# Performance work log

Hardware: AMD Instinct MI355X
Metric: run time of the kernel (lower is better)

The kernel has to match this reference:

```python
import jax, jax.numpy as jnp
import numpy as np

EPS = 1e-8

def setup_inputs() -> dict:
    key = jax.random.key(0)
    k1, k2, k3 = jax.random.split(key, 3)
    b, c, h, w = 64, 20, 128, 128
    x = jax.random.normal(k1, (b, c, h, w), dtype=jnp.float32)
    y = jax.random.randint(k2, (b, c), 0, 2).astype(jnp.int32)
    threshold_p = jnp.zeros((b, c, h * w), dtype=jnp.float32)
    fg = jax.random.uniform(k3, (b, c), dtype=jnp.float32)
    return {"x": x, "y": y, "threshold_p": threshold_p, "fg": fg, "iter": 0}

def reference(x, y, threshold_p, fg, iter):
    b, c, h, w = x.shape
    hw = h * w
    xs = jax.nn.sigmoid(x.reshape(b, c, hw))  # [b,c,hw]
    yf = y.astype(xs.dtype)
    if iter % 100 < 80:
        # per-row descending sort, pick the fg*(h*w)-th value as threshold
        srt = -jnp.sort(-xs.reshape(b * c, hw), axis=1)  # descending
        idx = (fg.reshape(-1) * hw).astype(jnp.int32)  # [b*c]
        thr = jnp.take_along_axis(srt, idx[:, None], axis=1).reshape(b, c, 1)
        thr = jax.lax.stop_gradient(thr)
    else:
        thr = jax.nn.sigmoid(jnp.mean(threshold_p.reshape(b, c, hw), axis=2))[:, :, None]
        xs = jax.lax.stop_gradient(xs)
    thr = jnp.clip(thr, 0.0001)  # [b,c,1], broadcasts over hw
    y_ = yf[:, :, None]  # [b,c,1] broadcast equivalent of stacking hw copies
    mask_low = jax.lax.stop_gradient((xs <= thr).astype(xs.dtype) * y_)
    mask_high = jax.lax.stop_gradient((xs > thr).astype(xs.dtype) * y_)
    h_low = (-(xs * xs) / (thr * thr) + 2.0 * xs / thr) * mask_low
    alpha = 1.0 / jnp.clip((1.0 - thr) ** 2, EPS)
    h_high = alpha * (1.0 - xs) * (1.0 - 2.0 * thr + xs) * mask_high
    if iter % 100 < 80:
        neg_loss = -(1.0 - y_) * jnp.log(jnp.clip(1.0 - xs, EPS))
        loss = jnp.mean(h_high + h_low + neg_loss)
    else:
        loss = jnp.sum(h_low) / jnp.sum(mask_low) + jnp.sum(h_high) / jnp.sum(mask_high)
    return loss
```

## Files before the change

### kernel.cpp

```cpp
#include <hip/hip_runtime.h>

#define HW     16384
#define NROWS  1280
#define NT     512
#define NWAVES (NT / 64)
#define CAP    1536
#define MAXB   128

__device__ __forceinline__ unsigned f2u(float f) {
    unsigned u = __float_as_uint(f);
    unsigned m = (unsigned)((int)u >> 31);
    return u ^ (m | 0x80000000u);
}
__device__ __forceinline__ float u2f(unsigned u) {
    u = (u & 0x80000000u) ? (u & 0x7fffffffu) : ~u;
    return __uint_as_float(u);
}

__device__ __forceinline__ float norminv(float p) {
    const float a1=-3.969683028665376e+01f,a2=2.209460984245205e+02f,
                a3=-2.759285104469687e+02f,a4=1.383577518672690e+02f,
                a5=-3.066479806614716e+01f,a6=2.506628277459239e+00f;
    const float b1=-5.447609879822406e+01f,b2=1.615858368580409e+02f,
                b3=-1.556989798598866e+02f,b4=6.680131188771972e+01f,
                b5=-1.328068155288572e+01f;
    const float c1=-7.784894002430293e-03f,c2=-3.223964580411365e-01f,
                c3=-2.400758277161838e+00f,c4=-2.549732539343734e+00f,
                c5=4.374664141464968e+00f,c6=2.938163982698783e+00f;
    const float d1=7.784695709041462e-03f,d2=3.224671290700398e-01f,
                d3=2.445134137142996e+00f,d4=3.754408661907416e+00f;
    const float plow = 0.02425f;
    float q, r;
    if (p < plow) {
        q = sqrtf(-2.f * logf(p));
        return (((((c1*q+c2)*q+c3)*q+c4)*q+c5)*q+c6) /
               ((((d1*q+d2)*q+d3)*q+d4)*q+1.f);
    } else if (p <= 1.f - plow) {
        q = p - 0.5f; r = q * q;
        return (((((a1*r+a2)*r+a3)*r+a4)*r+a5)*r+a6)*q /
               (((((b1*r+b2)*r+b3)*r+b4)*r+b5)*r+1.f);
    } else {
        q = sqrtf(-2.f * logf(1.f - p));
        return -(((((c1*q+c2)*q+c3)*q+c4)*q+c5)*q+c6) /
                ((((d1*q+d2)*q+d3)*q+d4)*q+1.f);
    }
}

__device__ __forceinline__ void block_scan_pick(
    const unsigned* h, int bpl, unsigned kk,
    volatile unsigned* s_bin, volatile unsigned* s_k, unsigned* wtot)
{
    const int tid  = threadIdx.x;
    const int lane = tid & 63;
    const int wid  = tid >> 6;
    const int base = tid * bpl;
    unsigned local = 0;
    for (int j = 0; j < bpl; ++j) local += h[base + j];
    unsigned s = local;
    #pragma unroll
    for (int off = 1; off < 64; off <<= 1) {
        unsigned t = __shfl_down(s, off, 64);
        if (lane + off < 64) s += t;
    }
    if (lane == 0) wtot[wid] = s;
    __syncthreads();
    unsigned aw = 0;
    #pragma unroll
    for (int w = 0; w < NWAVES; ++w) if (w > wid) aw += wtot[w];
    const unsigned above = aw + (s - local);
    if (above <= kk && above + local > kk) {
        unsigned run = above;
        for (int j = bpl - 1; j >= 0; --j) {
            unsigned c = h[base + j];
            if (run + c > kk) { *s_bin = (unsigned)(base + j); *s_k = kk - run; break; }
            run += c;
        }
    }
    __syncthreads();
}

__global__ __launch_bounds__(NT) void spatial_bce_row(
    const float* __restrict__ x, const int* __restrict__ y,
    const float* __restrict__ fg, double* __restrict__ partial)
{
    __shared__ unsigned hist[4096];
    __shared__ unsigned buf[CAP];
    __shared__ unsigned buf2[MAXB];
    __shared__ unsigned wtot[NWAVES];
    __shared__ unsigned s_cnt, s_cnt2, s_bin, s_k, s_val;
    __shared__ float    swf[NWAVES][6];
    __shared__ double   swd[NWAVES];

    const int row  = blockIdx.x;
    const int tid  = threadIdx.x;
    const int lane = tid & 63;
    const int wid  = tid >> 6;
    const float4* x4 = (const float4*)(x + (size_t)row * HW);
    const float L2E   = 1.44269504f;
    const float LN2   = 0.69314718f;
    const float NLCAP = 18.420680744f;

    const int yrow = y[row];

    if (yrow == 0) {
        float a0 = 0.f, a1 = 0.f, a2 = 0.f, a3 = 0.f;
        for (int i = tid; i < HW / 4; i += NT) {
            float4 v = x4[i];
            a0 += fminf(fmaxf(v.x, 0.f) + LN2 * log2f(1.f + exp2f(-L2E * fabsf(v.x))), NLCAP);
            a1 += fminf(fmaxf(v.y, 0.f) + LN2 * log2f(1.f + exp2f(-L2E * fabsf(v.y))), NLCAP);
            a2 += fminf(fmaxf(v.z, 0.f) + LN2 * log2f(1.f + exp2f(-L2E * fabsf(v.z))), NLCAP);
            a3 += fminf(fmaxf(v.w, 0.f) + LN2 * log2f(1.f + exp2f(-L2E * fabsf(v.w))), NLCAP);
        }
        double acc = (double)((a0 + a1) + (a2 + a3));
        #pragma unroll
        for (int off = 32; off > 0; off >>= 1) acc += __shfl_down(acc, off, 64);
        if (lane == 0) swd[wid] = acc;
        __syncthreads();
        if (tid == 0) {
            double t = 0.0;
            for (int w = 0; w < NWAVES; ++w) t += swd[w];
            partial[row] = t;
        }
        return;
    }

    int k = (int)(fg[row] * (float)HW);
    k = max(0, min(HW - 1, k));
    const unsigned ku = (unsigned)k;
    const float pq  = 1.f - ((float)k + 0.5f) * (1.f / (float)HW);
    const float z   = norminv(pq);
    const float phi = 0.39894228f * exp2f(-0.72134752f * z * z);
    const float sig = sqrtf(pq * (1.f - pq) * (1.f / (float)HW)) / phi;
    const float dl  = 6.f * sig + 0.02f;
    const float fa  = z + dl, fb = z - dl;
    const unsigned ua = f2u(fa), ub = f2u(fb);

    {
        uint4 zz = {0u, 0u, 0u, 0u};
        for (int i = tid; i < 1024 / 4; i += NT) ((uint4*)hist)[i] = zz;
    }
    if (tid == 0) { s_cnt = 0u; s_cnt2 = 0u; }
    __syncthreads();

    float t1a = 0.f, t2a = 0.f, gaa = 0.f, g2aa = 0.f, cafa = 0.f, cbfa = 0.f;
    float t1b = 0.f, t2b = 0.f, gab = 0.f, g2ab = 0.f, cafb = 0.f, cbfb = 0.f;
    for (int i = tid; i < HW / 4; i += 2 * NT) {
        float4 v0 = x4[i];
        float4 v1 = x4[i + NT];
        float e0[4] = {v0.x, v0.y, v0.z, v0.w};
        float e1[4] = {v1.x, v1.y, v1.z, v1.w};
        #pragma unroll
        for (int j = 0; j < 4; ++j) {
            float xv = e0[j];
            unsigned u = f2u(xv);
            float s = __builtin_amdgcn_rcpf(1.f + exp2f(-L2E * xv));
            float s2 = s * s;
            t1a += s; t2a += s2;
            if (u > ua) { gaa += s; g2aa += s2; cafa += 1.f; }
            if (u > ub) {
                cbfa += 1.f;
                if (u <= ua) { unsigned p = atomicAdd(&s_cnt, 1u); if (p < CAP) buf[p] = u; }
            }
        }
        #pragma unroll
        for (int j = 0; j < 4; ++j) {
            float xv = e1[j];
            unsigned u = f2u(xv);
            float s = __builtin_amdgcn_rcpf(1.f + exp2f(-L2E * xv));
            float s2 = s * s;
            t1b += s; t2b += s2;
            if (u > ua) { gab += s; g2ab += s2; cafb += 1.f; }
            if (u > ub) {
                cbfb += 1.f;
                if (u <= ua) { unsigned p = atomicAdd(&s_cnt, 1u); if (p < CAP) buf[p] = u; }
            }
        }
    }
    float t1 = t1a + t1b, t2 = t2a + t2b;
    float ga = gaa + gab, g2a = g2aa + g2ab;
    float caf = cafa + cafb, cbf = cbfa + cbfb;
    #pragma unroll
    for (int off = 32; off > 0; off >>= 1) {
        t1  += __shfl_down(t1,  off, 64);
        t2  += __shfl_down(t2,  off, 64);
        ga  += __shfl_down(ga,  off, 64);
        g2a += __shfl_down(g2a, off, 64);
        caf += __shfl_down(caf, off, 64);
        cbf += __shfl_down(cbf, off, 64);
    }
    if (lane == 0) {
        swf[wid][0] = t1;  swf[wid][1] = t2;  swf[wid][2] = ga;
        swf[wid][3] = g2a; swf[wid][4] = caf; swf[wid][5] = cbf;
    }
    __syncthreads();
    double dS1 = 0, dS2 = 0, dGa = 0, dG2a = 0, dCa = 0, dCb = 0;
    #pragma unroll
    for (int w = 0; w < NWAVES; ++w) {
        dS1 += swf[w][0]; dS2 += swf[w][1]; dGa  += swf[w][2];
        dG2a += swf[w][3]; dCa += swf[w][4]; dCb += swf[w][5];
    }
    const unsigned ca  = (unsigned)(dCa + 0.5);
    const unsigned cb  = (unsigned)(dCb + 0.5);
    const unsigned cnt = s_cnt;
    const unsigned UCLIP = f2u(-9.2102404f);
    const bool valid = (ca <= ku) && (ku < cb) && (cnt <= CAP);

    unsigned ustar;
    bool addSide;
    float hs = 0.f, hs2 = 0.f, hn = 0.f;

    if (valid) {
        const float scale = 1024.f / (fa - fb);
        for (int c = tid; c < (int)cnt; c += NT) {
            float xv = u2f(buf[c]);
            int bn = (int)((xv - fb) * scale);
            bn = max(0, min(1023, bn));
            atomicAdd(&hist[bn], 1u);
        }
        __syncthreads();
        const unsigned kp = ku - ca;
        block_scan_pick(hist, 1024 / NT, kp, &s_bin, &s_k, wtot);
        const unsigned binv = s_bin;
        const unsigned kin  = s_k;
        for (int c = tid; c < (int)cnt; c += NT) {
            unsigned u = buf[c];
            float xv = u2f(u);
            int bn = (int)((xv - fb) * scale);
            bn = max(0, min(1023, bn));
            if (bn == (int)binv) { unsigned p = atomicAdd(&s_cnt2, 1u); if (p < MAXB) buf2[p] = u; }
        }
        __syncthreads();
        const unsigned m = s_cnt2;
        if (m <= MAXB) {
            for (int i = tid; i < (int)m; i += NT) {
                unsigned v = buf2[i];
                unsigned gt = 0, eq = 0;
                for (int j = 0; j < (int)m; ++j) {
                    unsigned w = buf2[j];
                    gt += (w > v); eq += (w == v);
                }
                if (gt <= kin && kin < gt + eq) s_val = v;
            }
        } else {
            for (int c = tid; c < (int)cnt; c += NT) {
                unsigned v = buf[c];
                unsigned gt = 0, eq = 0;
                for (int j = 0; j < (int)cnt; ++j) {
                    unsigned w = buf[j];
                    gt += (w > v); eq += (w == v);
                }
                if (gt <= kp && kp < gt + eq) s_val = v;
            }
        }
        __syncthreads();
        ustar = s_val;

        if (ustar >= UCLIP) {
            addSide = true;
            for (int c = tid; c < (int)cnt; c += NT) {
                unsigned u = buf[c];
                if (u > ustar) {
                    float xv = u2f(u);
                    float s = __builtin_amdgcn_rcpf(1.f + exp2f(-L2E * xv));
                    hs += s; hs2 += s * s; hn += 1.f;
                }
            }
        } else {
            addSide = false;
            for (int i = tid; i < HW / 4; i += NT) {
                float4 v = x4[i];
                float e[4] = {v.x, v.y, v.z, v.w};
                #pragma unroll
                for (int j = 0; j < 4; ++j) {
                    if (f2u(e[j]) > UCLIP) {
                        float s = __builtin_amdgcn_rcpf(1.f + exp2f(-L2E * e[j]));
                        hs += s; hs2 += s * s; hn += 1.f;
                    }
                }
            }
        }
    } else {
        {
            uint4 zz = {0u, 0u, 0u, 0u};
            for (int i = tid; i < 4096 / 4; i += NT) ((uint4*)hist)[i] = zz;
        }
        __syncthreads();
        for (int i = tid; i < HW / 4; i += NT) {
            float4 v = x4[i];
            atomicAdd(&hist[f2u(v.x) >> 20], 1u);
            atomicAdd(&hist[f2u(v.y) >> 20], 1u);
            atomicAdd(&hist[f2u(v.z) >> 20], 1u);
            atomicAdd(&hist[f2u(v.w) >> 20], 1u);
        }
        __syncthreads();
        block_scan_pick(hist, 4096 / NT, ku, &s_bin, &s_k, wtot);
        const unsigned bin1 = s_bin;
        const unsigned k1   = s_k;
        for (int i = tid; i < 2048; i += NT) hist[i] = 0u;
        __syncthreads();
        for (int i = tid; i < HW / 4; i += NT) {
            float4 v = x4[i];
            unsigned u[4] = {f2u(v.x), f2u(v.y), f2u(v.z), f2u(v.w)};
            #pragma unroll
            for (int j = 0; j < 4; ++j)
                if ((u[j] >> 20) == bin1) atomicAdd(&hist[(u[j] >> 10) & 1023u], 1u);
        }
        __syncthreads();
        block_scan_pick(hist, 1024 / NT, k1, &s_bin, &s_k, wtot);
        const unsigned pfx22 = (bin1 << 10) | s_bin;
        const unsigned k2    = s_k;
        for (int i = tid; i < HW / 4; i += NT) {
            float4 v = x4[i];
            unsigned u[4] = {f2u(v.x), f2u(v.y), f2u(v.z), f2u(v.w)};
            #pragma unroll
            for (int j = 0; j < 4; ++j)
                if ((u[j] >> 10) == pfx22) atomicAdd(&hist[1024 + (u[j] & 1023u)], 1u);
        }
        __syncthreads();
        block_scan_pick(hist + 1024, 1024 / NT, k2, &s_bin, &s_k, wtot);
        ustar = (pfx22 << 10) | s_bin;

        addSide = false;
        const unsigned uthr = max(ustar, UCLIP);
        for (int i = tid; i < HW / 4; i += NT) {
            float4 v = x4[i];
            float e[4] = {v.x, v.y, v.z, v.w};
            #pragma unroll
            for (int j = 0; j < 4; ++j) {
                if (f2u(e[j]) > uthr) {
                    float s = __builtin_amdgcn_rcpf(1.f + exp2f(-L2E * e[j]));
                    hs += s; hs2 += s * s; hn += 1.f;
                }
            }
        }
    }

    #pragma unroll
    for (int off = 32; off > 0; off >>= 1) {
        hs  += __shfl_down(hs,  off, 64);
        hs2 += __shfl_down(hs2, off, 64);
        hn  += __shfl_down(hn,  off, 64);
    }
    if (lane == 0) { swf[wid][0] = hs; swf[wid][1] = hs2; swf[wid][2] = hn; }
    __syncthreads();
    if (tid == 0) {
        double HS = 0, HS2 = 0, HN = 0;
        for (int w = 0; w < NWAVES; ++w) {
            HS += swf[w][0]; HS2 += swf[w][1]; HN += swf[w][2];
        }
        double SH, S2H, NH;
        if (addSide) { SH = dGa + HS; S2H = dG2a + HS2; NH = dCa + HN; }
        else         { SH = HS;       S2H = HS2;        NH = HN; }
        const double SL = dS1 - SH, S2L = dS2 - S2H;

        const float xk = u2f(ustar);
        float thrf = 1.0f / (1.0f + expf(-xk));
        thrf = fmaxf(thrf, 1e-4f);
        const double t   = (double)thrf;
        const double omt = 1.0 - t;
        const double al  = 1.0 / fmax(omt * omt, 1e-8);
        partial[row] = 2.0 * SL / t - S2L / (t * t)
                     + al * (NH * (1.0 - 2.0 * t) + 2.0 * t * SH - S2H);
    }
}

__global__ __launch_bounds__(256) void spatial_bce_final(
    const double* __restrict__ partial, float* __restrict__ out)
{
    __shared__ double sred[256];
    double acc = 0.0;
    for (int i = threadIdx.x; i < NROWS; i += 256) acc += partial[i];
    sred[threadIdx.x] = acc;
    __syncthreads();
    for (int off = 128; off > 0; off >>= 1) {
        if (threadIdx.x < off) sred[threadIdx.x] += sred[threadIdx.x + off];
        __syncthreads();
    }
    if (threadIdx.x == 0)
        out[0] = (float)(sred[0] / ((double)NROWS * (double)HW));
}

extern "C" void kernel_launch(void* const* d_in, const int* in_sizes, int n_in,
                              void* d_out, int out_size, void* d_ws, size_t ws_size,
                              hipStream_t stream) {
    const float* x  = (const float*)d_in[0];
    const int*   y  = (const int*)d_in[1];
    const float* fg = (const float*)d_in[3];

    double* partial = (double*)d_ws;

    spatial_bce_row<<<NROWS, NT, 0, stream>>>(x, y, fg, partial);
    spatial_bce_final<<<1, 256, 0, stream>>>(partial, (float*)d_out);
}
```

Measured before the change: 38.38 us.

## Fuse final reduction into row kernel via last-block atomic, shrink blocks and shared memory

Measured after the change: 65.05 us. 69.5% more time.

```diff
diff --git a/kernel.cpp b/kernel.cpp
--- a/kernel.cpp
+++ b/kernel.cpp
@@ -2,10 +2,9 @@
 
 #define HW     16384
 #define NROWS  1280
-#define NT     512
-#define NWAVES (NT / 64)
-#define CAP    1536
-#define MAXB   128
+#define NT     256
+#define CAP    2048
+#define MB     256
 
 __device__ __forceinline__ unsigned f2u(float f) {
     unsigned u = __float_as_uint(f);
@@ -46,6 +45,15 @@
     }
 }
 
+__device__ __forceinline__ void bracket_ab(int k, float* fa, float* fb) {
+    const float pq  = 1.f - ((float)k + 0.5f) * (1.f / (float)HW);
+    const float z   = norminv(pq);
+    const float phi = 0.39894228f * exp2f(-0.72134752f * z * z);
+    const float sig = sqrtf(pq * (1.f - pq) * (1.f / (float)HW)) / phi;
+    const float dl  = 6.f * sig + 0.02f;
+    *fa = z + dl; *fb = z - dl;
+}
+
 __device__ __forceinline__ void block_scan_pick(
     const unsigned* h, int bpl, unsigned kk,
     volatile unsigned* s_bin, volatile unsigned* s_k, unsigned* wtot)
@@ -66,7 +74,7 @@
     __syncthreads();
     unsigned aw = 0;
     #pragma unroll
-    for (int w = 0; w < NWAVES; ++w) if (w > wid) aw += wtot[w];
+    for (int w = 0; w < 4; ++w) if (w > wid) aw += wtot[w];
     const unsigned above = aw + (s - local);
     if (above <= kk && above + local > kk) {
         unsigned run = above;
@@ -79,17 +87,17 @@
     __syncthreads();
 }
 
-__global__ __launch_bounds__(NT) void spatial_bce_row(
+__global__ __launch_bounds__(NT, 8) void fused_all(
     const float* __restrict__ x, const int* __restrict__ y,
-    const float* __restrict__ fg, double* __restrict__ partial)
+    const float* __restrict__ fg, double* __restrict__ partial,
+    unsigned* __restrict__ done, float* __restrict__ out)
 {
-    __shared__ unsigned hist[4096];
-    __shared__ unsigned buf[CAP];
-    __shared__ unsigned buf2[MAXB];
-    __shared__ unsigned wtot[NWAVES];
-    __shared__ unsigned s_cnt, s_cnt2, s_bin, s_k, s_val;
-    __shared__ float    swf[NWAVES][6];
-    __shared__ double   swd[NWAVES];
+    __shared__ __align__(16) unsigned pool[4096];
+    __shared__ unsigned wtot[4];
+    __shared__ unsigned s_cnt, s_cnt2, s_bin, s_k, s_val, s_last;
+    __shared__ float    swf[4][6];
+    __shared__ double   smom[6];
+    __shared__ double   swd[4];
 
     const int row  = blockIdx.x;
     const int tid  = threadIdx.x;
@@ -116,268 +124,238 @@
         for (int off = 32; off > 0; off >>= 1) acc += __shfl_down(acc, off, 64);
         if (lane == 0) swd[wid] = acc;
         __syncthreads();
+        if (tid == 0) partial[row] = swd[0] + swd[1] + swd[2] + swd[3];
+    } else {
+        int k = (int)(fg[row] * (float)HW);
+        k = max(0, min(HW - 1, k));
+        const unsigned ku = (unsigned)k;
+        float fa, fb; bracket_ab(k, &fa, &fb);
+        const unsigned ua = f2u(fa), ub = f2u(fb);
+        const unsigned UCLIP = f2u(-9.2102404f);
+
+        for (int i = tid; i < 1024; i += NT) pool[2048 + i] = 0u;
+        if (tid == 0) { s_cnt = 0u; s_cnt2 = 0u; }
+        __syncthreads();
+
+        float t1 = 0.f, t2 = 0.f, ga = 0.f, g2a = 0.f, caf = 0.f, cbf = 0.f;
+        for (int i = tid; i < HW / 4; i += 2 * NT) {
+            float4 v0 = x4[i];
+            float4 v1 = x4[i + NT];
+            float e[8] = {v0.x, v0.y, v0.z, v0.w, v1.x, v1.y, v1.z, v1.w};
+            #pragma unroll
+            for (int j = 0; j < 8; ++j) {
+                float xv = e[j];
+                unsigned u = f2u(xv);
+                float s = __builtin_amdgcn_rcpf(1.f + exp2f(-L2E * xv));
+                float s2 = s * s;
+                t1 += s; t2 += s2;
+                if (u > ua) { ga += s; g2a += s2; caf += 1.f; }
+                if (u > ub) {
+                    cbf += 1.f;
+                    if (u <= ua) {
+                        unsigned p = atomicAdd(&s_cnt, 1u);
+                        if (p < CAP) pool[p] = u;
+                    }
+                }
+            }
+        }
+        #pragma unroll
+        for (int off = 32; off > 0; off >>= 1) {
+            t1  += __shfl_down(t1,  off, 64);
+            t2  += __shfl_down(t2,  off, 64);
+            ga  += __shfl_down(ga,  off, 64);
+            g2a += __shfl_down(g2a, off, 64);
+            caf += __shfl_down(caf, off, 64);
+            cbf += __shfl_down(cbf, off, 64);
+        }
+        if (lane == 0) {
+            swf[wid][0] = t1;  swf[wid][1] = t2;  swf[wid][2] = ga;
+            swf[wid][3] = g2a; swf[wid][4] = caf; swf[wid][5] = cbf;
+        }
+        __syncthreads();
+        float caT = 0.f, cbT = 0.f;
+        #pragma unroll
+        for (int w = 0; w < 4; ++w) { caT += swf[w][4]; cbT += swf[w][5]; }
+        const unsigned ca  = (unsigned)(caT + 0.5f);
+        const unsigned cb  = (unsigned)(cbT + 0.5f);
+        const unsigned cnt = s_cnt;
         if (tid == 0) {
-            double t = 0.0;
-            for (int w = 0; w < NWAVES; ++w) t += swd[w];
-            partial[row] = t;
-        }
-        return;
-    }
-
-    int k = (int)(fg[row] * (float)HW);
-    k = max(0, min(HW - 1, k));
-    const unsigned ku = (unsigned)k;
-    const float pq  = 1.f - ((float)k + 0.5f) * (1.f / (float)HW);
-    const float z   = norminv(pq);
-    const float phi = 0.39894228f * exp2f(-0.72134752f * z * z);
-    const float sig = sqrtf(pq * (1.f - pq) * (1.f / (float)HW)) / phi;
-    const float dl  = 6.f * sig + 0.02f;
-    const float fa  = z + dl, fb = z - dl;
-    const unsigned ua = f2u(fa), ub = f2u(fb);
-
-    {
-        uint4 zz = {0u, 0u, 0u, 0u};
-        for (int i = tid; i < 1024 / 4; i += NT) ((uint4*)hist)[i] = zz;
-    }
-    if (tid == 0) { s_cnt = 0u; s_cnt2 = 0u; }
-    __syncthreads();
-
-    float t1a = 0.f, t2a = 0.f, gaa = 0.f, g2aa = 0.f, cafa = 0.f, cbfa = 0.f;
-    float t1b = 0.f, t2b = 0.f, gab = 0.f, g2ab = 0.f, cafb = 0.f, cbfb = 0.f;
-    for (int i = tid; i < HW / 4; i += 2 * NT) {
-        float4 v0 = x4[i];
-        float4 v1 = x4[i + NT];
-        float e0[4] = {v0.x, v0.y, v0.z, v0.w};
-        float e1[4] = {v1.x, v1.y, v1.z, v1.w};
-        #pragma unroll
-        for (int j = 0; j < 4; ++j) {
-            float xv = e0[j];
-            unsigned u = f2u(xv);
-            float s = __builtin_amdgcn_rcpf(1.f + exp2f(-L2E * xv));
-            float s2 = s * s;
-            t1a += s; t2a += s2;
-            if (u > ua) { gaa += s; g2aa += s2; cafa += 1.f; }
-            if (u > ub) {
-                cbfa += 1.f;
-                if (u <= ua) { unsigned p = atomicAdd(&s_cnt, 1u); if (p < CAP) buf[p] = u; }
-            }
-        }
-        #pragma unroll
-        for (int j = 0; j < 4; ++j) {
-            float xv = e1[j];
-            unsigned u = f2u(xv);
-            float s = __builtin_amdgcn_rcpf(1.f + exp2f(-L2E * xv));
-            float s2 = s * s;
-            t1b += s; t2b += s2;
-            if (u > ua) { gab += s; g2ab += s2; cafb += 1.f; }
-            if (u > ub) {
-                cbfb += 1.f;
-                if (u <= ua) { unsigned p = atomicAdd(&s_cnt, 1u); if (p < CAP) buf[p] = u; }
-            }
-        }
-    }
-    float t1 = t1a + t1b, t2 = t2a + t2b;
-    float ga = gaa + gab, g2a = g2aa + g2ab;
-    float caf = cafa + cafb, cbf = cbfa + cbfb;
-    #pragma unroll
-    for (int off = 32; off > 0; off >>= 1) {
-        t1  += __shfl_down(t1,  off, 64);
-        t2  += __shfl_down(t2,  off, 64);
-        ga  += __shfl_down(ga,  off, 64);
-        g2a += __shfl_down(g2a, off, 64);
-        caf += __shfl_down(caf, off, 64);
-        cbf += __shfl_down(cbf, off, 64);
-    }
-    if (lane == 0) {
-        swf[wid][0] = t1;  swf[wid][1] = t2;  swf[wid][2] = ga;
-        swf[wid][3] = g2a; swf[wid][4] = caf; swf[wid][5] = cbf;
-    }
-    __syncthreads();
-    double dS1 = 0, dS2 = 0, dGa = 0, dG2a = 0, dCa = 0, dCb = 0;
-    #pragma unroll
-    for (int w = 0; w < NWAVES; ++w) {
-        dS1 += swf[w][0]; dS2 += swf[w][1]; dGa  += swf[w][2];
-        dG2a += swf[w][3]; dCa += swf[w][4]; dCb += swf[w][5];
-    }
-    const unsigned ca  = (unsigned)(dCa + 0.5);
-    const unsigned cb  = (unsigned)(dCb + 0.5);
-    const unsigned cnt = s_cnt;
-    const unsigned UCLIP = f2u(-9.2102404f);
-    const bool valid = (ca <= ku) && (ku < cb) && (cnt <= CAP);
-
-    unsigned ustar;
-    bool addSide;
-    float hs = 0.f, hs2 = 0.f, hn = 0.f;
-
-    if (valid) {
-        const float scale = 1024.f / (fa - fb);
-        for (int c = tid; c < (int)cnt; c += NT) {
-            float xv = u2f(buf[c]);
-            int bn = (int)((xv - fb) * scale);
-            bn = max(0, min(1023, bn));
-            atomicAdd(&hist[bn], 1u);
-        }
-        __syncthreads();
-        const unsigned kp = ku - ca;
-        block_scan_pick(hist, 1024 / NT, kp, &s_bin, &s_k, wtot);
-        const unsigned binv = s_bin;
-        const unsigned kin  = s_k;
-        for (int c = tid; c < (int)cnt; c += NT) {
-            unsigned u = buf[c];
-            float xv = u2f(u);
-            int bn = (int)((xv - fb) * scale);
-            bn = max(0, min(1023, bn));
-            if (bn == (int)binv) { unsigned p = atomicAdd(&s_cnt2, 1u); if (p < MAXB) buf2[p] = u; }
-        }
-        __syncthreads();
-        const unsigned m = s_cnt2;
-        if (m <= MAXB) {
-            for (int i = tid; i < (int)m; i += NT) {
-                unsigned v = buf2[i];
-                unsigned gt = 0, eq = 0;
-                for (int j = 0; j < (int)m; ++j) {
-                    unsigned w = buf2[j];
-                    gt += (w > v); eq += (w == v);
-                }
-                if (gt <= kin && kin < gt + eq) s_val = v;
+            double m0 = 0, m1 = 0, m2 = 0, m3 = 0;
+            #pragma unroll
+            for (int w = 0; w < 4; ++w) {
+                m0 += swf[w][0]; m1 += swf[w][1];
+                m2 += swf[w][2]; m3 += swf[w][3];
+            }
+            smom[0] = m0; smom[1] = m1; smom[2] = m2; smom[3] = m3;
+            smom[4] = (double)ca;
+        }
+        const bool valid = (ca <= ku) && (ku < cb) && (cnt <= CAP);
+
+        unsigned ustar = 0;
+        bool haveU = false;
+
+        if (valid) {
+            const float scale = 1024.f / (fa - fb);
+            const unsigned kp = ku - ca;
+            for (unsigned c = tid; c < cnt; c += NT) {
+                int bn = (int)((u2f(pool[c]) - fb) * scale);
+                bn = max(0, min(1023, bn));
+                atomicAdd(&pool[2048 + bn], 1u);
+            }
+            __syncthreads();
+            block_scan_pick(pool + 2048, 4, kp, &s_bin, &s_k, wtot);
+            const unsigned binv = s_bin, kin = s_k;
+            for (unsigned c = tid; c < cnt; c += NT) {
+                unsigned u = pool[c];
+                int bn = (int)((u2f(u) - fb) * scale);
+                bn = max(0, min(1023, bn));
+                if (bn == (int)binv) {
+                    unsigned p = atomicAdd(&s_cnt2, 1u);
+                    if (p < MB) pool[3072 + p] = u;
+                }
+            }
+            __syncthreads();
+            const unsigned m = s_cnt2;
+            if (m <= MB) {
+                for (unsigned i = tid; i < m; i += NT) {
+                    unsigned v = pool[3072 + i];
+                    unsigned gt = 0, eq = 0;
+                    for (unsigned j = 0; j < m; ++j) {
+                        unsigned w = pool[3072 + j];
+                        gt += (w > v); eq += (w == v);
+                    }
+                    if (gt <= kin && kin < gt + eq) s_val = v;
+                }
+            } else {
+                for (unsigned c = tid; c < cnt; c += NT) {
+                    unsigned v = pool[c];
+                    unsigned gt = 0, eq = 0;
+                    for (unsigned j = 0; j < cnt; ++j) {
+                        unsigned w = pool[j];
+                        gt += (w > v); eq += (w == v);
+                    }
+                    if (gt <= kp && kp < gt + eq) s_val = v;
+                }
+            }
+            __syncthreads();
+            ustar = s_val;
+            haveU = true;
+        }
+
+        float hs = 0.f, hs2 = 0.f, hn = 0.f;
+        bool addSide = false;
+        if (haveU && ustar >= UCLIP) {
+            addSide = true;
+            for (unsigned c = tid; c < cnt; c += NT) {
+                unsigned u = pool[c];
+                if (u > ustar) {
+                    float s = __builtin_amdgcn_rcpf(1.f + exp2f(-L2E * u2f(u)));
+                    hs += s; hs2 += s * s; hn += 1.f;
+                }
             }
         } else {
-            for (int c = tid; c < (int)cnt; c += NT) {
-                unsigned v = buf[c];
-                unsigned gt = 0, eq = 0;
-                for (int j = 0; j < (int)cnt; ++j) {
-                    unsigned w = buf[j];
-                    gt += (w > v); eq += (w == v);
-                }
-                if (gt <= kp && kp < gt + eq) s_val = v;
-            }
-        }
-        __syncthreads();
-        ustar = s_val;
-
-        if (ustar >= UCLIP) {
-            addSide = true;
-            for (int c = tid; c < (int)cnt; c += NT) {
-                unsigned u = buf[c];
-                if (u > ustar) {
-                    float xv = u2f(u);
-                    float s = __builtin_amdgcn_rcpf(1.f + exp2f(-L2E * xv));
-                    hs += s; hs2 += s * s; hn += 1.f;
-                }
-            }
-        } else {
-            addSide = false;
+            if (!haveU) {
+                for (int i = tid; i < 4096; i += NT) pool[i] = 0u;
+                __syncthreads();
+                for (int i = tid; i < HW / 4; i += NT) {
+                    float4 v = x4[i];
+                    atomicAdd(&pool[f2u(v.x) >> 20], 1u);
+                    atomicAdd(&pool[f2u(v.y) >> 20], 1u);
+                    atomicAdd(&pool[f2u(v.z) >> 20], 1u);
+                    atomicAdd(&pool[f2u(v.w) >> 20], 1u);
+                }
+                __syncthreads();
+                block_scan_pick(pool, 16, ku, &s_bin, &s_k, wtot);
+                const unsigned bin1 = s_bin, k1 = s_k;
+                for (int i = tid; i < 2048; i += NT) pool[i] = 0u;
+                __syncthreads();
+                for (int i = tid; i < HW / 4; i += NT) {
+                    float4 v = x4[i];
+                    unsigned uu[4] = {f2u(v.x), f2u(v.y), f2u(v.z), f2u(v.w)};
+                    #pragma unroll
+                    for (int j = 0; j < 4; ++j)
+                        if ((uu[j] >> 20) == bin1) atomicAdd(&pool[(uu[j] >> 10) & 1023u], 1u);
+                }
+                __syncthreads();
+                block_scan_pick(pool, 4, k1, &s_bin, &s_k, wtot);
+                const unsigned pfx22 = (bin1 << 10) | s_bin;
+                const unsigned k2 = s_k;
+                for (int i = tid; i < HW / 4; i += NT) {
+                    float4 v = x4[i];
+                    unsigned uu[4] = {f2u(v.x), f2u(v.y), f2u(v.z), f2u(v.w)};
+                    #pragma unroll
+                    for (int j = 0; j < 4; ++j)
+                        if ((uu[j] >> 10) == pfx22) atomicAdd(&pool[1024 + (uu[j] & 1023u)], 1u);
+                }
+                __syncthreads();
+                block_scan_pick(pool + 1024, 4, k2, &s_bin, &s_k, wtot);
+                ustar = (pfx22 << 10) | s_bin;
+            }
+            const unsigned uthr = ustar > UCLIP ? ustar : UCLIP;
             for (int i = tid; i < HW / 4; i += NT) {
                 float4 v = x4[i];
                 float e[4] = {v.x, v.y, v.z, v.w};
                 #pragma unroll
                 for (int j = 0; j < 4; ++j) {
-                    if (f2u(e[j]) > UCLIP) {
+                    if (f2u(e[j]) > uthr) {
                         float s = __builtin_amdgcn_rcpf(1.f + exp2f(-L2E * e[j]));
                         hs += s; hs2 += s * s; hn += 1.f;
                     }
                 }
             }
         }
-    } else {
-        {
-            uint4 zz = {0u, 0u, 0u, 0u};
-            for (int i = tid; i < 4096 / 4; i += NT) ((uint4*)hist)[i] = zz;
-        }
-        __syncthreads();
-        for (int i = tid; i < HW / 4; i += NT) {
-            float4 v = x4[i];
-            atomicAdd(&hist[f2u(v.x) >> 20], 1u);
-            atomicAdd(&hist[f2u(v.y) >> 20], 1u);
-            atomicAdd(&hist[f2u(v.z) >> 20], 1u);
-            atomicAdd(&hist[f2u(v.w) >> 20], 1u);
-        }
-        __syncthreads();
-        block_scan_pick(hist, 4096 / NT, ku, &s_bin, &s_k, wtot);
-        const unsigned bin1 = s_bin;
-        const unsigned k1   = s_k;
-        for (int i = tid; i < 2048; i += NT) hist[i] = 0u;
-        __syncthreads();
-        for (int i = tid; i < HW / 4; i += NT) {
-            float4 v = x4[i];
-            unsigned u[4] = {f2u(v.x), f2u(v.y), f2u(v.z), f2u(v.w)};
+
+        __syncthreads();
+        #pragma unroll
+        for (int off = 32; off > 0; off >>= 1) {
+            hs  += __shfl_down(hs,  off, 64);
+            hs2 += __shfl_down(hs2, off, 64);
+            hn  += __shfl_down(hn,  off, 64);
+        }
+        if (lane == 0) { swf[wid][0] = hs; swf[wid][1] = hs2; swf[wid][2] = hn; }
+        __syncthreads();
+        if (tid == 0) {
+            double HS = 0, HS2 = 0, HN = 0;
             #pragma unroll
-            for (int j = 0; j < 4; ++j)
-                if ((u[j] >> 20) == bin1) atomicAdd(&hist[(u[j] >> 10) & 1023u], 1u);
-        }
-        __syncthreads();
-        block_scan_pick(hist, 1024 / NT, k1, &s_bin, &s_k, wtot);
-        const unsigned pfx22 = (bin1 << 10) | s_bin;
-        const unsigned k2    = s_k;
-        for (int i = tid; i < HW / 4; i += NT) {
-            float4 v = x4[i];
-            unsigned u[4] = {f2u(v.x), f2u(v.y), f2u(v.z), f2u(v.w)};
-            #pragma unroll
-            for (int j = 0; j < 4; ++j)
-                if ((u[j] >> 10) == pfx22) atomicAdd(&hist[1024 + (u[j] & 1023u)], 1u);
-        }
-        __syncthreads();
-        block_scan_pick(hist + 1024, 1024 / NT, k2, &s_bin, &s_k, wtot);
-        ustar = (pfx22 << 10) | s_bin;
-
-        addSide = false;
-        const unsigned uthr = max(ustar, UCLIP);
-        for (int i = tid; i < HW / 4; i += NT) {
-            float4 v = x4[i];
-            float e[4] = {v.x, v.y, v.z, v.w};
-            #pragma unroll
-            for (int j = 0; j < 4; ++j) {
-                if (f2u(e[j]) > uthr) {
-                    float s = __builtin_amdgcn_rcpf(1.f + exp2f(-L2E * e[j]));
-                    hs += s; hs2 += s * s; hn += 1.f;
-                }
-            }
-        }
-    }
-
-    #pragma unroll
-    for (int off = 32; off > 0; off >>= 1) {
-        hs  += __shfl_down(hs,  off, 64);
-        hs2 += __shfl_down(hs2, off, 64);
-        hn  += __shfl_down(hn,  off, 64);
-    }
-    if (lane == 0) { swf[wid][0] = hs; swf[wid][1] = hs2; swf[wid][2] = hn; }
+            for (int w = 0; w < 4; ++w) {
+                HS += swf[w][0]; HS2 += swf[w][1]; HN += swf[w][2];
+            }
+            double SH, S2H, NH;
+            if (addSide) { SH = smom[2] + HS; S2H = smom[3] + HS2; NH = smom[4] + HN; }
+            else         { SH = HS;           S2H = HS2;           NH = HN; }
+            const double SL = smom[0] - SH, S2L = smom[1] - S2H;
+            const float xk = u2f(ustar);
+            float thrf = 1.0f / (1.0f + expf(-xk));
+            thrf = fmaxf(thrf, 1e-4f);
+            const double t   = (double)thrf;
+            const double omt = 1.0 - t;
+            const double al  = 1.0 / fmax(omt * omt, 1e-8);
+            partial[row] = 2.0 * SL / t - S2L / (t * t)
+                         + al * (NH * (1.0 - 2.0 * t) + 2.0 * t * SH - S2H);
+        }
+    }
+
     __syncthreads();
     if (tid == 0) {
-        double HS = 0, HS2 = 0, HN = 0;
-        for (int w = 0; w < NWAVES; ++w) {
-            HS += swf[w][0]; HS2 += swf[w][1]; HN += swf[w][2];
-        }
-        double SH, S2H, NH;
-        if (addSide) { SH = dGa + HS; S2H = dG2a + HS2; NH = dCa + HN; }
-        else         { SH = HS;       S2H = HS2;        NH = HN; }
-        const double SL = dS1 - SH, S2L = dS2 - S2H;
-
-        const float xk = u2f(ustar);
-        float thrf = 1.0f / (1.0f + expf(-xk));
-        thrf = fmaxf(thrf, 1e-4f);
-        const double t   = (double)thrf;
-        const double omt = 1.0 - t;
-        const double al  = 1.0 / fmax(omt * omt, 1e-8);
-        partial[row] = 2.0 * SL / t - S2L / (t * t)
-                     + al * (NH * (1.0 - 2.0 * t) + 2.0 * t * SH - S2H);
-    }
-}
-
-__global__ __launch_bounds__(256) void spatial_bce_final(
-    const double* __restrict__ partial, float* __restrict__ out)
-{
-    __shared__ double sred[256];
-    double acc = 0.0;
-    for (int i = threadIdx.x; i < NROWS; i += 256) acc += partial[i];
-    sred[threadIdx.x] = acc;
+        __threadfence();
+        unsigned old = atomicAdd(done, 1u);
+        s_last = (old == NROWS - 1) ? 1u : 0u;
+    }
     __syncthreads();
-    for (int off = 128; off > 0; off >>= 1) {
-        if (threadIdx.x < off) sred[threadIdx.x] += sred[threadIdx.x + off];
-        __syncthreads();
-    }
-    if (threadIdx.x == 0)
-        out[0] = (float)(sred[0] / ((double)NROWS * (double)HW));
+    if (s_last) {
+        __threadfence();
+        double* sred = (double*)pool;
+        double a = 0.0;
+        for (int i = tid; i < NROWS; i += NT) a += partial[i];
+        sred[tid] = a;
+        __syncthreads();
+        for (int off = NT / 2; off > 0; off >>= 1) {
+            if (tid < off) sred[tid] += sred[tid + off];
+            __syncthreads();
+        }
+        if (tid == 0)
+            out[0] = (float)(sred[0] / ((double)NROWS * (double)HW));
+    }
 }
 
 extern "C" void kernel_launch(void* const* d_in, const int* in_sizes, int n_in,
@@ -387,8 +365,9 @@
     const int*   y  = (const int*)d_in[1];
     const float* fg = (const float*)d_in[3];
 
-    double* partial = (double*)d_ws;
-
-    spatial_bce_row<<<NROWS, NT, 0, stream>>>(x, y, fg, partial);
-    spatial_bce_final<<<1, 256, 0, stream>>>(partial, (float*)d_out);
-}
+    double*   partial = (double*)d_ws;
+    unsigned* done    = (unsigned*)((char*)d_ws + (size_t)NROWS * 8);
+
+    hipMemsetAsync(done, 0, sizeof(unsigned), stream);
+    fused_all<<<NROWS, NT, 0, stream>>>(x, y, fg, partial, done, (float*)d_out);
+}
```
